# Kernel tuning notes

Measured on AMD Instinct MI355X. Metric: run time of the kernel, lower is better.

Reference implementation:

```python
import jax, jax.numpy as jnp
import numpy as np

B = 1024
N_CPGS = 20000
N_FREQS = N_CPGS // 2 + 1  # 10001
HIDDEN = (256, 128, 64)
LN_EPS = 1e-5


def setup_inputs() -> dict:
    key = jax.random.key(0)
    keys = jax.random.split(key, 16)
    inp = {"x": jax.random.normal(keys[0], (B, N_CPGS), dtype=jnp.float32)}
    in_dim = N_FREQS
    for i, h in enumerate(HIDDEN):
        inp[f"W{i}"] = jax.random.normal(keys[1 + i], (h, in_dim), dtype=jnp.float32) * 0.01
        inp[f"alpha{i}"] = jnp.full((h, in_dim), 0.01, dtype=jnp.float32)
        inp[f"b{i}"] = jnp.zeros((h,), dtype=jnp.float32)
        inp[f"eta{i}"] = jnp.asarray(0.1, dtype=jnp.float32)
        inp[f"g{i}"] = jnp.ones((h,), dtype=jnp.float32)   # LayerNorm gamma
        inp[f"be{i}"] = jnp.zeros((h,), dtype=jnp.float32)  # LayerNorm beta
        in_dim = h
    inp["head_w"] = jax.random.normal(keys[10], (1, in_dim), dtype=jnp.float32) * (1.0 / np.sqrt(in_dim))
    inp["head_b"] = jnp.zeros((1,), dtype=jnp.float32)
    return inp


def _hebbian_layer(x, W, alpha, b, eta):
    # y_slow = x W^T + b;  plastic[b,i] = eta * tanh(y_slow)[b,i] * sum_j sigmoid(alpha)[i,j] * x_norm[b,j] * x[b,j]
    y_slow = jnp.einsum('bd,hd->bh', x, W) + b
    x_norm = x / (jnp.linalg.norm(x, axis=-1, keepdims=True) + 1e-8)
    c = x_norm * x  # (B, in) -- collapses the (B,out,in) outer-product trace algebraically
    plastic = eta * jnp.tanh(y_slow) * jnp.einsum('bd,hd->bh', c, jax.nn.sigmoid(alpha))
    return y_slow + plastic


def _layer_norm(h, g, be):
    mu = jnp.mean(h, axis=-1, keepdims=True)
    var = jnp.mean((h - mu) ** 2, axis=-1, keepdims=True)
    return (h - mu) * jax.lax.rsqrt(var + LN_EPS) * g + be


def reference(x, W0, alpha0, b0, eta0, g0, be0,
              W1, alpha1, b1, eta1, g1, be1,
              W2, alpha2, b2, eta2, g2, be2,
              head_w, head_b):
    # FFT spectral front-end
    xc = x - jnp.mean(x, axis=1, keepdims=True)
    h = jnp.log1p(jnp.abs(jnp.fft.rfft(xc, axis=1)))  # (B, N_FREQS)
    params = [(W0, alpha0, b0, eta0, g0, be0),
              (W1, alpha1, b1, eta1, g1, be1),
              (W2, alpha2, b2, eta2, g2, be2)]
    for (W, a, b, eta, g, be) in params:
        h = jax.nn.gelu(_layer_norm(_hebbian_layer(h, W, a, b, eta), g, be), approximate=False)
        # dropout is identity in eval mode
    return (jnp.einsum('bd,od->bo', h, head_w) + head_b)[:, 0]  # (B,)
```

## Files before the change

### kernel.cpp

```cpp
#include <hip/hip_runtime.h>
#include <hip/hip_bf16.h>
#include <math.h>

typedef short bf16x8 __attribute__((ext_vector_type(8)));
typedef float f32x4 __attribute__((ext_vector_type(4)));

static __device__ __forceinline__ unsigned short f2bf(float f) {
    unsigned int u = __float_as_uint(f);
    unsigned int r = (u + 0x7fffu + ((u >> 16) & 1u)) >> 16;
    return (unsigned short)r;
}

static __device__ __forceinline__ bf16x8 sq_bf16x8(bf16x8 a) {
    bf16x8 r;
    #pragma unroll
    for (int i = 0; i < 8; ++i) {
        unsigned int u = ((unsigned int)(unsigned short)a[i]) << 16;
        float f = __uint_as_float(u);
        f *= f;
        r[i] = (short)f2bf(f);
    }
    return r;
}

static __device__ __forceinline__ float gelu_f(float x) {
    return 0.5f * x * (1.f + erff(x * 0.70710678118654752f));
}

static __device__ __forceinline__ void gload_lds16(const void* g, void* l) {
    __builtin_amdgcn_global_load_lds(
        (const __attribute__((address_space(1))) unsigned int*)g,
        (__attribute__((address_space(3))) unsigned int*)l, 16, 0, 0);
}

static __device__ __forceinline__ int ldsmap(int i) { return i + (i >> 6); }

static __device__ __forceinline__ int rev4(int k) {
    int d0 = k % 10; k /= 10;
    int d1 = k % 10; k /= 10;
    int d2 = k % 10; int d3 = k / 10;
    return d0 * 1000 + d1 * 100 + d2 * 10 + d3;
}

static __device__ __forceinline__ void dft5(
    float a0r, float a0i, float a1r, float a1i, float a2r, float a2i,
    float a3r, float a3i, float a4r, float a4i,
    float* Xr, float* Xi)
{
    const float c1 = 0.30901699437494742f, c2 = -0.80901699437494745f;
    const float s1 = 0.95105651629515357f, s2 = 0.58778525229247312f;
    float t1r = a1r + a4r, t1i = a1i + a4i;
    float d1r = a1r - a4r, d1i = a1i - a4i;
    float t2r = a2r + a3r, t2i = a2i + a3i;
    float d2r = a2r - a3r, d2i = a2i - a3i;
    Xr[0] = a0r + t1r + t2r; Xi[0] = a0i + t1i + t2i;
    float m1r = a0r + c1 * t1r + c2 * t2r, m1i = a0i + c1 * t1i + c2 * t2i;
    float m2r = a0r + c2 * t1r + c1 * t2r, m2i = a0i + c2 * t1i + c1 * t2i;
    float n1r = s1 * d1r + s2 * d2r, n1i = s1 * d1i + s2 * d2i;
    float n2r = s2 * d1r - s1 * d2r, n2i = s2 * d1i - s1 * d2i;
    Xr[1] = m1r + n1i; Xi[1] = m1i - n1r;
    Xr[4] = m1r - n1i; Xi[4] = m1i + n1r;
    Xr[2] = m2r + n2i; Xi[2] = m2i - n2r;
    Xr[3] = m2r - n2i; Xi[3] = m2i + n2r;
}

template<int S>
static __device__ __forceinline__ void radix10_stage(
    float* __restrict__ reb, float* __restrict__ imb, int tid, float mean)
{
    constexpr int L  = (S == 0) ? 1000 : (S == 1) ? 100 : (S == 2) ? 10 : 1;
    constexpr int SC = (S == 0) ? 1 : (S == 1) ? 10 : (S == 2) ? 100 : 1000;
    constexpr bool TW = (S != 3);

    const float WR[5] = {1.f, 0.80901699437494745f, 0.30901699437494742f,
                         -0.30901699437494742f, -0.80901699437494745f};
    const float WI[5] = {0.f, -0.58778525229247312f, -0.95105651629515357f,
                         -0.95105651629515357f, -0.58778525229247312f};

    for (int w = tid; w < 1000; w += 512) {
        int g, j;
        if (S == 0)      { g = 0; j = w; }
        else if (S == 3) { g = w; j = 0; }
        else             { g = w / L; j = w - g * L; }
        const int base = g * (10 * L) + j;

        float ar[10], ai[10];
        #pragma unroll
        for (int u = 0; u < 10; ++u) {
            int idx = ldsmap(base + u * L);
            ar[u] = reb[idx];
            ai[u] = imb[idx];
        }
        if (S == 0) {
            #pragma unroll
            for (int u = 0; u < 10; ++u) { ar[u] -= mean; ai[u] -= mean; }
        }

        float Er[5], Ei[5], Or[5], Oi[5];
        dft5(ar[0], ai[0], ar[2], ai[2], ar[4], ai[4], ar[6], ai[6], ar[8], ai[8], Er, Ei);
        dft5(ar[1], ai[1], ar[3], ai[3], ar[5], ai[5], ar[7], ai[7], ar[9], ai[9], Or, Oi);
        #pragma unroll
        for (int k = 1; k < 5; ++k) {
            float tr = Or[k] * WR[k] - Oi[k] * WI[k];
            Oi[k] = Or[k] * WI[k] + Oi[k] * WR[k];
            Or[k] = tr;
        }

        if (TW) {
            const float ang = (float)(j * SC) * -6.28318530717958648e-4f;
            float w1c, w1s;
            __sincosf(ang, &w1s, &w1c);
            float twr[10], twi[10];
            twr[0] = 1.f; twi[0] = 0.f;
            #pragma unroll
            for (int t = 1; t < 10; ++t) {
                twr[t] = twr[t - 1] * w1c - twi[t - 1] * w1s;
                twi[t] = twr[t - 1] * w1s + twi[t - 1] * w1c;
            }
            #pragma unroll
            for (int k = 0; k < 5; ++k) {
                float xr0 = Er[k] + Or[k], xi0 = Ei[k] + Oi[k];
                float xr1 = Er[k] - Or[k], xi1 = Ei[k] - Oi[k];
                int i0 = ldsmap(base + k * L);
                int i1 = ldsmap(base + (k + 5) * L);
                if (k == 0) {
                    reb[i0] = xr0;
                    imb[i0] = xi0;
                } else {
                    reb[i0] = xr0 * twr[k] - xi0 * twi[k];
                    imb[i0] = xr0 * twi[k] + xi0 * twr[k];
                }
                reb[i1] = xr1 * twr[k + 5] - xi1 * twi[k + 5];
                imb[i1] = xr1 * twi[k + 5] + xi1 * twr[k + 5];
            }
        } else {
            #pragma unroll
            for (int k = 0; k < 5; ++k) {
                int i0 = ldsmap(base + k * L);
                int i1 = ldsmap(base + (k + 5) * L);
                reb[i0] = Er[k] + Or[k]; imb[i0] = Ei[k] + Oi[k];
                reb[i1] = Er[k] - Or[k]; imb[i1] = Ei[k] - Oi[k];
            }
        }
    }
}

__global__ __launch_bounds__(512, 4)
void fft_prep_kernel(const float* __restrict__ x,
                     unsigned short* __restrict__ hb,
                     float* __restrict__ hnorm,
                     const float* __restrict__ W0, const float* __restrict__ A0,
                     unsigned short* __restrict__ Wb, unsigned short* __restrict__ Sb,
                     const float* __restrict__ W1, const float* __restrict__ A1,
                     const float* __restrict__ W2, const float* __restrict__ A2,
                     float* __restrict__ W1T, float* __restrict__ S1T,
                     float* __restrict__ W2T, float* __restrict__ S2T)
{
    if (blockIdx.x >= 1024) {
        int idx = (blockIdx.x - 1024) * 512 + threadIdx.x;
        if (idx < 1280128) {
            const bool isW = idx < 640064;
            const int f4 = isW ? idx : idx - 640064;
            const float* src = isW ? W0 : A0;
            unsigned short* dst = isW ? Wb : Sb;
            float4 v = ((const float4*)src)[f4];
            float e[4] = {v.x, v.y, v.z, v.w};
            int flat = f4 * 4;
            int row = flat / 10001;
            int col = flat - row * 10001;
            #pragma unroll
            for (int i = 0; i < 4; ++i) {
                if (col == 10001) { row++; col = 0; }
                float val = isW ? e[i] : 1.f / (1.f + expf(-e[i]));
                dst[(size_t)row * 10240 + col] = f2bf(val);
                col++;
            }
        } else if (idx < 1341312) {
            int i = idx - 1280128;
            int row = i / 239;
            int col = 10001 + (i - row * 239);
            Wb[(size_t)row * 10240 + col] = 0;
            Sb[(size_t)row * 10240 + col] = 0;
        } else if (idx < 1423232) {
            int o = idx - 1341312;
            if (o < 32768) {
                int d = o >> 7, h = o & 127;
                W1T[o] = W1[h * 256 + d];
            } else if (o < 65536) {
                int p = o - 32768;
                int d = p >> 7, h = p & 127;
                S1T[p] = 1.f / (1.f + expf(-A1[h * 256 + d]));
            } else if (o < 73728) {
                int p = o - 65536;
                int d = p >> 6, h = p & 63;
                W2T[p] = W2[h * 128 + d];
            } else {
                int p = o - 73728;
                int d = p >> 6, h = p & 63;
                S2T[p] = 1.f / (1.f + expf(-A2[h * 128 + d]));
            }
        }
        return;
    }

    __shared__ float reb[10156];
    __shared__ float imb[10156];
    __shared__ float redbuf[8];

    const int b = blockIdx.x;
    const int tid = threadIdx.x;
    const int lane = tid & 63;
    const int wv = tid >> 6;
    const float* xr = x + (size_t)b * 20000;

    float sum = 0.f;
    for (int i4 = tid; i4 < 5000; i4 += 512) {
        float4 v = ((const float4*)xr)[i4];
        sum += v.x + v.y + v.z + v.w;
        int n = i4 * 2;
        reb[ldsmap(n)]     = v.x; imb[ldsmap(n)]     = v.y;
        reb[ldsmap(n + 1)] = v.z; imb[ldsmap(n + 1)] = v.w;
    }
    #pragma unroll
    for (int o = 32; o; o >>= 1) sum += __shfl_xor(sum, o);
    __syncthreads();
    if (lane == 0) redbuf[wv] = sum;
    __syncthreads();
    float tot = 0.f;
    #pragma unroll
    for (int i = 0; i < 8; ++i) tot += redbuf[i];
    const float mean = tot * (1.f / 20000.f);

    radix10_stage<0>(reb, imb, tid, mean);
    __syncthreads();
    radix10_stage<1>(reb, imb, tid, 0.f);
    __syncthreads();
    radix10_stage<2>(reb, imb, tid, 0.f);
    __syncthreads();
    radix10_stage<3>(reb, imb, tid, 0.f);
    __syncthreads();

    float sumsq = 0.f;
    unsigned short* hrow = hb + (size_t)b * 10240;
    #pragma unroll
    for (int i = 0; i < 20; ++i) {
        int k = tid + i * 512;
        float hval = 0.f;
        if (k <= 10000) {
            int k1 = (k == 10000) ? 0 : k;
            int k2 = (10000 - k) % 10000;
            int i1 = ldsmap(rev4(k1));
            int i2 = ldsmap(rev4(k2));
            float zr = reb[i1], zi = imb[i1];
            float wr = reb[i2], wi = imb[i2];
            float er = 0.5f * (zr + wr);
            float ei = 0.5f * (zi - wi);
            float odr = 0.5f * (zi + wi);
            float odi = -0.5f * (zr - wr);
            float ct, st;
            __sincosf((float)k * -3.14159265358979324e-4f, &st, &ct);
            float xre = er + ct * odr - st * odi;
            float xim = ei + ct * odi + st * odr;
            hval = log1pf(sqrtf(xre * xre + xim * xim));
        }
        hrow[k] = f2bf(hval);
        sumsq += hval * hval;
    }
    #pragma unroll
    for (int o = 32; o; o >>= 1) sumsq += __shfl_xor(sumsq, o);
    __syncthreads();
    if (lane == 0) redbuf[wv] = sumsq;
    __syncthreads();
    if (tid == 0) {
        float tsq = 0.f;
        #pragma unroll
        for (int i = 0; i < 8; ++i) tsq += redbuf[i];
        hnorm[b] = 1.f / (sqrtf(tsq) + 1e-8f);
    }
}

__global__ __launch_bounds__(256, 2)
void gemm0_kernel(const unsigned short* __restrict__ hb,
                  const unsigned short* __restrict__ Wb, const unsigned short* __restrict__ Sb,
                  float* __restrict__ Py, float* __restrict__ Pp)
{
    __shared__ unsigned short Ah[128 * 64];
    __shared__ unsigned short Bw[64 * 64];
    __shared__ unsigned short Bs[64 * 64];

    const int t = threadIdx.x;
    const int b0 = blockIdx.x * 128;
    const int n0 = blockIdx.y * 64;
    const int z = blockIdx.z;
    const int lane = t & 63;
    const int wv = t >> 6;
    const int ml = lane & 15;
    const int q4 = lane >> 4;
    const int s0 = q4 ^ (ml & 7);

    const int sub = lane >> 3;
    const int sl = lane & 7;
    const int gsw = sl ^ sub;

    f32x4 accY[2][4], accP[2][4];
    #pragma unroll
    for (int mt = 0; mt < 2; ++mt)
        #pragma unroll
        for (int nt = 0; nt < 4; ++nt) {
            accY[mt][nt] = (f32x4){0.f, 0.f, 0.f, 0.f};
            accP[mt][nt] = (f32x4){0.f, 0.f, 0.f, 0.f};
        }

    const int kbase = z * 640;

    for (int step = 0; step < 10; ++step) {
        const int k0 = kbase + step * 64;
        __syncthreads();
        #pragma unroll
        for (int j = 0; j < 4; ++j) {
            const int c = wv * 4 + j;
            const size_t go = (size_t)(b0 + c * 8 + sub) * 10240 + k0 + gsw * 8;
            gload_lds16(&hb[go], &Ah[c * 512]);
        }
        #pragma unroll
        for (int j = 0; j < 2; ++j) {
            const int c = wv * 2 + j;
            const size_t go = (size_t)(n0 + c * 8 + sub) * 10240 + k0 + gsw * 8;
            gload_lds16(&Wb[go], &Bw[c * 512]);
            gload_lds16(&Sb[go], &Bs[c * 512]);
        }
        __syncthreads();

        #pragma unroll
        for (int kk = 0; kk < 2; ++kk) {
            const int slot = (s0 ^ (kk << 2)) << 3;
            bf16x8 ah[2], ac[2], bw[4], bs[4];
            #pragma unroll
            for (int mt = 0; mt < 2; ++mt) {
                int mrow = wv * 32 + mt * 16 + ml;
                ah[mt] = *(const bf16x8*)&Ah[mrow * 64 + slot];
                ac[mt] = sq_bf16x8(ah[mt]);
            }
            #pragma unroll
            for (int nt = 0; nt < 4; ++nt) {
                int nrow = nt * 16 + ml;
                bw[nt] = *(const bf16x8*)&Bw[nrow * 64 + slot];
                bs[nt] = *(const bf16x8*)&Bs[nrow * 64 + slot];
            }
            #pragma unroll
            for (int mt = 0; mt < 2; ++mt)
                #pragma unroll
                for (int nt = 0; nt < 4; ++nt) {
                    accY[mt][nt] = __builtin_amdgcn_mfma_f32_16x16x32_bf16(ah[mt], bw[nt], accY[mt][nt], 0, 0, 0);
                    accP[mt][nt] = __builtin_amdgcn_mfma_f32_16x16x32_bf16(ac[mt], bs[nt], accP[mt][nt], 0, 0, 0);
                }
        }
    }

    const int rq = q4 * 4;
    #pragma unroll
    for (int mt = 0; mt < 2; ++mt)
        #pragma unroll
        for (int nt = 0; nt < 4; ++nt)
            #pragma unroll
            for (int r = 0; r < 4; ++r) {
                int m = b0 + wv * 32 + mt * 16 + rq + r;
                int n = n0 + nt * 16 + ml;
                size_t o = ((size_t)z * 1024 + m) * 256 + n;
                Py[o] = accY[mt][nt][r];
                Pp[o] = accP[mt][nt][r];
            }
}

__global__ __launch_bounds__(256)
void combine0_kernel(const float* __restrict__ Py, const float* __restrict__ Pp,
                     const float* __restrict__ hnorm,
                     const float* __restrict__ b0v, const float* __restrict__ eta0p,
                     const float* __restrict__ g0, const float* __restrict__ be0,
                     float* __restrict__ h1, float* __restrict__ c1)
{
    __shared__ float red[4];
    const int b = blockIdx.x;
    const int h = threadIdx.x;
    const int lane = h & 63;
    const int wv = h >> 6;

    float ys = 0.f, ps = 0.f;
    for (int s = 0; s < 16; ++s) {
        size_t o = ((size_t)s * 1024 + b) * 256 + h;
        ys += Py[o];
        ps += Pp[o];
    }
    ps *= hnorm[b];
    float y = ys + b0v[h];
    float v = y + eta0p[0] * tanhf(y) * ps;

    float s1 = v;
    #pragma unroll
    for (int o = 32; o; o >>= 1) s1 += __shfl_xor(s1, o);
    __syncthreads();
    if (lane == 0) red[wv] = s1;
    __syncthreads();
    float sum = red[0] + red[1] + red[2] + red[3];

    float s2 = v * v;
    #pragma unroll
    for (int o = 32; o; o >>= 1) s2 += __shfl_xor(s2, o);
    __syncthreads();
    if (lane == 0) red[wv] = s2;
    __syncthreads();
    float sumsq = red[0] + red[1] + red[2] + red[3];

    float mu = sum * (1.f / 256.f);
    float var = sumsq * (1.f / 256.f) - mu * mu;
    float u = (v - mu) * rsqrtf(var + 1e-5f) * g0[h] + be0[h];
    float gl = gelu_f(u);

    float s3 = gl * gl;
    #pragma unroll
    for (int o = 32; o; o >>= 1) s3 += __shfl_xor(s3, o);
    __syncthreads();
    if (lane == 0) red[wv] = s3;
    __syncthreads();
    float gsq = red[0] + red[1] + red[2] + red[3];
    float inv = 1.f / (sqrtf(gsq) + 1e-8f);

    h1[(size_t)b * 256 + h] = gl;
    c1[(size_t)b * 256 + h] = gl * gl * inv;
}

__global__ __launch_bounds__(256)
void tail_kernel(const float* __restrict__ h1, const float* __restrict__ c1,
                 const float* __restrict__ W1T, const float* __restrict__ S1T,
                 const float* __restrict__ b1, const float* __restrict__ eta1p,
                 const float* __restrict__ g1, const float* __restrict__ be1,
                 const float* __restrict__ W2T, const float* __restrict__ S2T,
                 const float* __restrict__ b2, const float* __restrict__ eta2p,
                 const float* __restrict__ g2, const float* __restrict__ be2,
                 const float* __restrict__ hw, const float* __restrict__ hbod,
                 float* __restrict__ out)
{
    __shared__ float sh[4][256];
    __shared__ float sc[4][256];
    __shared__ float sv[4][128];
    __shared__ float sh2[4][128];
    __shared__ float sc2[4][128];
    __shared__ float sv2[4][64];

    const int t = threadIdx.x;
    const int b0 = blockIdx.x * 4;
    const int lane = t & 63;
    const int wv = t >> 6;

    #pragma unroll
    for (int i = 0; i < 4; ++i) {
        int idx = t + i * 256;
        int r = idx >> 8, d = idx & 255;
        sh[r][d] = h1[(size_t)(b0 + r) * 256 + d];
        sc[r][d] = c1[(size_t)(b0 + r) * 256 + d];
    }
    __syncthreads();

    const int hcol = t & 127;
    const int r2 = t >> 7;
    float ya[2] = {0.f, 0.f};
    float pa[2] = {0.f, 0.f};
    for (int d = 0; d < 256; ++d) {
        float w = W1T[d * 128 + hcol];
        float s = S1T[d * 128 + hcol];
        #pragma unroll
        for (int i = 0; i < 2; ++i) {
            int r = r2 * 2 + i;
            ya[i] += sh[r][d] * w;
            pa[i] += sc[r][d] * s;
        }
    }
    const float e1 = eta1p[0];
    #pragma unroll
    for (int i = 0; i < 2; ++i) {
        int r = r2 * 2 + i;
        float y = ya[i] + b1[hcol];
        sv[r][hcol] = y + e1 * tanhf(y) * pa[i];
    }
    __syncthreads();

    {
        int r = wv;
        float v0 = sv[r][lane];
        float v1 = sv[r][lane + 64];
        float s = v0 + v1, sq = v0 * v0 + v1 * v1;
        #pragma unroll
        for (int o = 32; o; o >>= 1) { s += __shfl_xor(s, o); sq += __shfl_xor(sq, o); }
        float mu = s * (1.f / 128.f);
        float var = sq * (1.f / 128.f) - mu * mu;
        float rs = rsqrtf(var + 1e-5f);
        float u0 = (v0 - mu) * rs * g1[lane] + be1[lane];
        float u1 = (v1 - mu) * rs * g1[lane + 64] + be1[lane + 64];
        float ge0 = gelu_f(u0);
        float ge1 = gelu_f(u1);
        float gsq = ge0 * ge0 + ge1 * ge1;
        #pragma unroll
        for (int o = 32; o; o >>= 1) gsq += __shfl_xor(gsq, o);
        float inv = 1.f / (sqrtf(gsq) + 1e-8f);
        sh2[r][lane] = ge0; sh2[r][lane + 64] = ge1;
        sc2[r][lane] = ge0 * ge0 * inv; sc2[r][lane + 64] = ge1 * ge1 * inv;
    }
    __syncthreads();

    const int h2c = t & 63;
    const int r4 = t >> 6;
    float yb = 0.f, pb = 0.f;
    for (int d = 0; d < 128; ++d) {
        yb += sh2[r4][d] * W2T[d * 64 + h2c];
        pb += sc2[r4][d] * S2T[d * 64 + h2c];
    }
    {
        const float e2 = eta2p[0];
        float y = yb + b2[h2c];
        sv2[r4][h2c] = y + e2 * tanhf(y) * pb;
    }
    __syncthreads();

    {
        int r = wv;
        float v0 = sv2[r][lane];
        float s = v0, sq = v0 * v0;
        #pragma unroll
        for (int o = 32; o; o >>= 1) { s += __shfl_xor(s, o); sq += __shfl_xor(sq, o); }
        float mu = s * (1.f / 64.f);
        float var = sq * (1.f / 64.f) - mu * mu;
        float rs = rsqrtf(var + 1e-5f);
        float u = (v0 - mu) * rs * g2[lane] + be2[lane];
        float g = gelu_f(u);
        float hc = g * hw[lane];
        #pragma unroll
        for (int o = 32; o; o >>= 1) hc += __shfl_xor(hc, o);
        if (lane == 0) out[b0 + r] = hc + hbod[0];
    }
}

extern "C" void kernel_launch(void* const* d_in, const int* in_sizes, int n_in,
                              void* d_out, int out_size, void* d_ws, size_t ws_size,
                              hipStream_t stream)
{
    const float* x    = (const float*)d_in[0];
    const float* W0   = (const float*)d_in[1];
    const float* A0   = (const float*)d_in[2];
    const float* b0   = (const float*)d_in[3];
    const float* eta0 = (const float*)d_in[4];
    const float* g0   = (const float*)d_in[5];
    const float* be0  = (const float*)d_in[6];
    const float* W1   = (const float*)d_in[7];
    const float* A1   = (const float*)d_in[8];
    const float* b1   = (const float*)d_in[9];
    const float* eta1 = (const float*)d_in[10];
    const float* g1   = (const float*)d_in[11];
    const float* be1  = (const float*)d_in[12];
    const float* W2   = (const float*)d_in[13];
    const float* A2   = (const float*)d_in[14];
    const float* b2   = (const float*)d_in[15];
    const float* eta2 = (const float*)d_in[16];
    const float* g2   = (const float*)d_in[17];
    const float* be2  = (const float*)d_in[18];
    const float* hw   = (const float*)d_in[19];
    const float* hbod = (const float*)d_in[20];
    float* out = (float*)d_out;

    char* w = (char*)d_ws;
    unsigned short* hb  = (unsigned short*)(w + 0);
    unsigned short* Wb0 = (unsigned short*)(w + 20971520);
    unsigned short* Sb0 = (unsigned short*)(w + 26214400);
    float* Py   = (float*)(w + 31457280);
    float* Pp   = (float*)(w + 48234496);
    float* h1   = (float*)(w + 65011712);
    float* c1   = (float*)(w + 66060288);
    float* W1T  = (float*)(w + 67108864);
    float* S1T  = (float*)(w + 67239936);
    float* W2T  = (float*)(w + 67371008);
    float* S2T  = (float*)(w + 67403776);
    float* hnm  = (float*)(w + 67436544);

    hipLaunchKernelGGL(fft_prep_kernel, dim3(3804), dim3(512), 0, stream,
                       x, hb, hnm, W0, A0, Wb0, Sb0, W1, A1, W2, A2, W1T, S1T, W2T, S2T);
    hipLaunchKernelGGL(gemm0_kernel, dim3(8, 4, 16), dim3(256), 0, stream, hb, Wb0, Sb0, Py, Pp);
    hipLaunchKernelGGL(combine0_kernel, dim3(1024), dim3(256), 0, stream, Py, Pp, hnm, b0, eta0, g0, be0, h1, c1);
    hipLaunchKernelGGL(tail_kernel, dim3(256), dim3(256), 0, stream, h1, c1, W1T, S1T, b1, eta1, g1, be1,
                       W2T, S2T, b2, eta2, g2, be2, hw, hbod, out);
}
```

Baseline: 282.2 us.

## Process two FFT rows per 1024-thread block, sharing twiddles and index math

The FFT prep kernel now handles two batch rows per block of 1024 threads. Each of the 1000 active threads computes one butterfly position for both rows, so twiddle sincos, twiddle recurrences and LDS index maps are computed once and reused across the rows. The post-processing step also shares its sincos and indices across the two rows. The cost is double the shared memory per block (about 160 KB) and more register pressure, which can lower occupancy, and the side blocks for weight conversion now also run 1024 threads.

After: 294.0 us. 4.2% more time.

```diff
diff --git a/kernel.cpp b/kernel.cpp
--- a/kernel.cpp
+++ b/kernel.cpp
@@ -65,8 +65,9 @@
 }
 
 template<int S>
-static __device__ __forceinline__ void radix10_stage(
-    float* __restrict__ reb, float* __restrict__ imb, int tid, float mean)
+static __device__ __forceinline__ void radix10_stage2(
+    float (*__restrict__ reb)[10156], float (*__restrict__ imb)[10156],
+    int w, float mean0, float mean1)
 {
     constexpr int L  = (S == 0) ? 1000 : (S == 1) ? 100 : (S == 2) ? 10 : 1;
     constexpr int SC = (S == 0) ? 1 : (S == 1) ? 10 : (S == 2) ? 100 : 1000;
@@ -77,23 +78,37 @@
     const float WI[5] = {0.f, -0.58778525229247312f, -0.95105651629515357f,
                          -0.95105651629515357f, -0.58778525229247312f};
 
-    for (int w = tid; w < 1000; w += 512) {
-        int g, j;
-        if (S == 0)      { g = 0; j = w; }
-        else if (S == 3) { g = w; j = 0; }
-        else             { g = w / L; j = w - g * L; }
-        const int base = g * (10 * L) + j;
-
+    int g, j;
+    if (S == 0)      { g = 0; j = w; }
+    else if (S == 3) { g = w; j = 0; }
+    else             { g = w / L; j = w - g * L; }
+    const int base = g * (10 * L) + j;
+
+    int idx[10];
+    #pragma unroll
+    for (int u = 0; u < 10; ++u) idx[u] = ldsmap(base + u * L);
+
+    float twr[10], twi[10];
+    if (TW) {
+        const float ang = (float)(j * SC) * -6.28318530717958648e-4f;
+        float w1c, w1s;
+        __sincosf(ang, &w1s, &w1c);
+        twr[0] = 1.f; twi[0] = 0.f;
+        #pragma unroll
+        for (int t = 1; t < 10; ++t) {
+            twr[t] = twr[t - 1] * w1c - twi[t - 1] * w1s;
+            twi[t] = twr[t - 1] * w1s + twi[t - 1] * w1c;
+        }
+    }
+
+    #pragma unroll
+    for (int r = 0; r < 2; ++r) {
+        const float mm = (S == 0) ? (r ? mean1 : mean0) : 0.f;
         float ar[10], ai[10];
         #pragma unroll
         for (int u = 0; u < 10; ++u) {
-            int idx = ldsmap(base + u * L);
-            ar[u] = reb[idx];
-            ai[u] = imb[idx];
-        }
-        if (S == 0) {
-            #pragma unroll
-            for (int u = 0; u < 10; ++u) { ar[u] -= mean; ai[u] -= mean; }
+            ar[u] = reb[r][idx[u]] - mm;
+            ai[u] = imb[r][idx[u]] - mm;
         }
 
         float Er[5], Ei[5], Or[5], Oi[5];
@@ -107,45 +122,31 @@
         }
 
         if (TW) {
-            const float ang = (float)(j * SC) * -6.28318530717958648e-4f;
-            float w1c, w1s;
-            __sincosf(ang, &w1s, &w1c);
-            float twr[10], twi[10];
-            twr[0] = 1.f; twi[0] = 0.f;
-            #pragma unroll
-            for (int t = 1; t < 10; ++t) {
-                twr[t] = twr[t - 1] * w1c - twi[t - 1] * w1s;
-                twi[t] = twr[t - 1] * w1s + twi[t - 1] * w1c;
-            }
             #pragma unroll
             for (int k = 0; k < 5; ++k) {
                 float xr0 = Er[k] + Or[k], xi0 = Ei[k] + Oi[k];
                 float xr1 = Er[k] - Or[k], xi1 = Ei[k] - Oi[k];
-                int i0 = ldsmap(base + k * L);
-                int i1 = ldsmap(base + (k + 5) * L);
                 if (k == 0) {
-                    reb[i0] = xr0;
-                    imb[i0] = xi0;
+                    reb[r][idx[0]] = xr0;
+                    imb[r][idx[0]] = xi0;
                 } else {
-                    reb[i0] = xr0 * twr[k] - xi0 * twi[k];
-                    imb[i0] = xr0 * twi[k] + xi0 * twr[k];
+                    reb[r][idx[k]] = xr0 * twr[k] - xi0 * twi[k];
+                    imb[r][idx[k]] = xr0 * twi[k] + xi0 * twr[k];
                 }
-                reb[i1] = xr1 * twr[k + 5] - xi1 * twi[k + 5];
-                imb[i1] = xr1 * twi[k + 5] + xi1 * twr[k + 5];
+                reb[r][idx[k + 5]] = xr1 * twr[k + 5] - xi1 * twi[k + 5];
+                imb[r][idx[k + 5]] = xr1 * twi[k + 5] + xi1 * twr[k + 5];
             }
         } else {
             #pragma unroll
             for (int k = 0; k < 5; ++k) {
-                int i0 = ldsmap(base + k * L);
-                int i1 = ldsmap(base + (k + 5) * L);
-                reb[i0] = Er[k] + Or[k]; imb[i0] = Ei[k] + Oi[k];
-                reb[i1] = Er[k] - Or[k]; imb[i1] = Ei[k] - Oi[k];
-            }
-        }
-    }
-}
-
-__global__ __launch_bounds__(512, 4)
+                reb[r][idx[k]]     = Er[k] + Or[k]; imb[r][idx[k]]     = Ei[k] + Oi[k];
+                reb[r][idx[k + 5]] = Er[k] - Or[k]; imb[r][idx[k + 5]] = Ei[k] - Oi[k];
+            }
+        }
+    }
+}
+
+__global__ __launch_bounds__(1024)
 void fft_prep_kernel(const float* __restrict__ x,
                      unsigned short* __restrict__ hb,
                      float* __restrict__ hnorm,
@@ -156,8 +157,8 @@
                      float* __restrict__ W1T, float* __restrict__ S1T,
                      float* __restrict__ W2T, float* __restrict__ S2T)
 {
-    if (blockIdx.x >= 1024) {
-        int idx = (blockIdx.x - 1024) * 512 + threadIdx.x;
+    if (blockIdx.x >= 512) {
+        int idx = (blockIdx.x - 512) * 1024 + threadIdx.x;
         if (idx < 1280128) {
             const bool isW = idx < 640064;
             const int f4 = isW ? idx : idx - 640064;
@@ -203,79 +204,106 @@
         return;
     }
 
-    __shared__ float reb[10156];
-    __shared__ float imb[10156];
-    __shared__ float redbuf[8];
-
-    const int b = blockIdx.x;
+    __shared__ float reb[2][10156];
+    __shared__ float imb[2][10156];
+    __shared__ float redbuf[32];
+
     const int tid = threadIdx.x;
     const int lane = tid & 63;
     const int wv = tid >> 6;
-    const float* xr = x + (size_t)b * 20000;
-
+    const int half = tid >> 9;
+    const int t2 = tid & 511;
+    const int b0 = blockIdx.x * 2;
+
+    const float* xr = x + (size_t)(b0 + half) * 20000;
     float sum = 0.f;
-    for (int i4 = tid; i4 < 5000; i4 += 512) {
+    for (int i4 = t2; i4 < 5000; i4 += 512) {
         float4 v = ((const float4*)xr)[i4];
         sum += v.x + v.y + v.z + v.w;
         int n = i4 * 2;
-        reb[ldsmap(n)]     = v.x; imb[ldsmap(n)]     = v.y;
-        reb[ldsmap(n + 1)] = v.z; imb[ldsmap(n + 1)] = v.w;
+        reb[half][ldsmap(n)]     = v.x; imb[half][ldsmap(n)]     = v.y;
+        reb[half][ldsmap(n + 1)] = v.z; imb[half][ldsmap(n + 1)] = v.w;
     }
     #pragma unroll
     for (int o = 32; o; o >>= 1) sum += __shfl_xor(sum, o);
     __syncthreads();
     if (lane == 0) redbuf[wv] = sum;
     __syncthreads();
-    float tot = 0.f;
-    #pragma unroll
-    for (int i = 0; i < 8; ++i) tot += redbuf[i];
-    const float mean = tot * (1.f / 20000.f);
-
-    radix10_stage<0>(reb, imb, tid, mean);
-    __syncthreads();
-    radix10_stage<1>(reb, imb, tid, 0.f);
-    __syncthreads();
-    radix10_stage<2>(reb, imb, tid, 0.f);
-    __syncthreads();
-    radix10_stage<3>(reb, imb, tid, 0.f);
-    __syncthreads();
-
-    float sumsq = 0.f;
-    unsigned short* hrow = hb + (size_t)b * 10240;
-    #pragma unroll
-    for (int i = 0; i < 20; ++i) {
-        int k = tid + i * 512;
-        float hval = 0.f;
+    float tot0 = 0.f, tot1 = 0.f;
+    #pragma unroll
+    for (int i = 0; i < 8; ++i) { tot0 += redbuf[i]; tot1 += redbuf[8 + i]; }
+    const float mean0 = tot0 * (1.f / 20000.f);
+    const float mean1 = tot1 * (1.f / 20000.f);
+
+    if (tid < 1000) radix10_stage2<0>(reb, imb, tid, mean0, mean1);
+    __syncthreads();
+    if (tid < 1000) radix10_stage2<1>(reb, imb, tid, 0.f, 0.f);
+    __syncthreads();
+    if (tid < 1000) radix10_stage2<2>(reb, imb, tid, 0.f, 0.f);
+    __syncthreads();
+    if (tid < 1000) radix10_stage2<3>(reb, imb, tid, 0.f, 0.f);
+    __syncthreads();
+
+    float sq0 = 0.f, sq1 = 0.f;
+    unsigned short* hrow0 = hb + (size_t)b0 * 10240;
+    unsigned short* hrow1 = hrow0 + 10240;
+    #pragma unroll
+    for (int i = 0; i < 10; ++i) {
+        int k = tid + i * 1024;
         if (k <= 10000) {
             int k1 = (k == 10000) ? 0 : k;
-            int k2 = (10000 - k) % 10000;
+            int k2 = (10000 - k1) % 10000;
             int i1 = ldsmap(rev4(k1));
             int i2 = ldsmap(rev4(k2));
-            float zr = reb[i1], zi = imb[i1];
-            float wr = reb[i2], wi = imb[i2];
-            float er = 0.5f * (zr + wr);
-            float ei = 0.5f * (zi - wi);
-            float odr = 0.5f * (zi + wi);
-            float odi = -0.5f * (zr - wr);
             float ct, st;
             __sincosf((float)k * -3.14159265358979324e-4f, &st, &ct);
-            float xre = er + ct * odr - st * odi;
-            float xim = ei + ct * odi + st * odr;
-            hval = log1pf(sqrtf(xre * xre + xim * xim));
-        }
-        hrow[k] = f2bf(hval);
-        sumsq += hval * hval;
-    }
-    #pragma unroll
-    for (int o = 32; o; o >>= 1) sumsq += __shfl_xor(sumsq, o);
-    __syncthreads();
-    if (lane == 0) redbuf[wv] = sumsq;
+
+            {
+                float zr = reb[0][i1], zi = imb[0][i1];
+                float wr = reb[0][i2], wi = imb[0][i2];
+                float er = 0.5f * (zr + wr);
+                float ei = 0.5f * (zi - wi);
+                float odr = 0.5f * (zi + wi);
+                float odi = -0.5f * (zr - wr);
+                float xre = er + ct * odr - st * odi;
+                float xim = ei + ct * odi + st * odr;
+                float hv = log1pf(sqrtf(xre * xre + xim * xim));
+                hrow0[k] = f2bf(hv);
+                sq0 += hv * hv;
+            }
+            {
+                float zr = reb[1][i1], zi = imb[1][i1];
+                float wr = reb[1][i2], wi = imb[1][i2];
+                float er = 0.5f * (zr + wr);
+                float ei = 0.5f * (zi - wi);
+                float odr = 0.5f * (zi + wi);
+                float odi = -0.5f * (zr - wr);
+                float xre = er + ct * odr - st * odi;
+                float xim = ei + ct * odi + st * odr;
+                float hv = log1pf(sqrtf(xre * xre + xim * xim));
+                hrow1[k] = f2bf(hv);
+                sq1 += hv * hv;
+            }
+        } else {
+            hrow0[k] = 0;
+            hrow1[k] = 0;
+        }
+    }
+    #pragma unroll
+    for (int o = 32; o; o >>= 1) { sq0 += __shfl_xor(sq0, o); sq1 += __shfl_xor(sq1, o); }
+    __syncthreads();
+    if (lane == 0) { redbuf[wv] = sq0; redbuf[16 + wv] = sq1; }
     __syncthreads();
     if (tid == 0) {
-        float tsq = 0.f;
-        #pragma unroll
-        for (int i = 0; i < 8; ++i) tsq += redbuf[i];
-        hnorm[b] = 1.f / (sqrtf(tsq) + 1e-8f);
+        float t = 0.f;
+        #pragma unroll
+        for (int i = 0; i < 16; ++i) t += redbuf[i];
+        hnorm[b0] = 1.f / (sqrtf(t) + 1e-8f);
+    } else if (tid == 1) {
+        float t = 0.f;
+        #pragma unroll
+        for (int i = 0; i < 16; ++i) t += redbuf[16 + i];
+        hnorm[b0 + 1] = 1.f / (sqrtf(t) + 1e-8f);
     }
 }
 
@@ -580,7 +608,7 @@
     float* S2T  = (float*)(w + 67403776);
     float* hnm  = (float*)(w + 67436544);
 
-    hipLaunchKernelGGL(fft_prep_kernel, dim3(3804), dim3(512), 0, stream,
+    hipLaunchKernelGGL(fft_prep_kernel, dim3(1902), dim3(1024), 0, stream,
                        x, hb, hnm, W0, A0, Wb0, Sb0, W1, A1, W2, A2, W1T, S1T, W2T, S2T);
     hipLaunchKernelGGL(gemm0_kernel, dim3(8, 4, 16), dim3(256), 0, stream, hb, Wb0, Sb0, Py, Pp);
     hipLaunchKernelGGL(combine0_kernel, dim3(1024), dim3(256), 0, stream, Py, Pp, hnm, b0, eta0, g0, be0, h1, c1);
```

## Fuse layer-0 combine into tail kernel and use cheaper log in FFT

Applied to the files above, without the earlier changes.

Merges the split-K reduction, Hebbian combine, LayerNorm and GELU for layer 0 into the tail kernel. Each block now handles four rows, which removes one launch and the h1/c1 round trip through global memory. The FFT epilogue swaps the modulo for a branch and log1pf for __logf(1+x). The fused kernel uses only 256 blocks to read the split-K partials, and __logf(1+x) loses precision for small magnitudes.

Measured after the change: 266.0 us. 1.06x faster.

```diff
diff --git a/kernel.cpp b/kernel.cpp
--- a/kernel.cpp
+++ b/kernel.cpp
@@ -248,7 +248,7 @@
         float hval = 0.f;
         if (k <= 10000) {
             int k1 = (k == 10000) ? 0 : k;
-            int k2 = (10000 - k) % 10000;
+            int k2 = (k1 == 0) ? 0 : 10000 - k1;
             int i1 = ldsmap(rev4(k1));
             int i2 = ldsmap(rev4(k2));
             float zr = reb[i1], zi = imb[i1];
@@ -261,7 +261,7 @@
             __sincosf((float)k * -3.14159265358979324e-4f, &st, &ct);
             float xre = er + ct * odr - st * odi;
             float xim = ei + ct * odi + st * odr;
-            hval = log1pf(sqrtf(xre * xre + xim * xim));
+            hval = __logf(1.f + sqrtf(xre * xre + xim * xim));
         }
         hrow[k] = f2bf(hval);
         sumsq += hval * hval;
@@ -373,64 +373,10 @@
 }
 
 __global__ __launch_bounds__(256)
-void combine0_kernel(const float* __restrict__ Py, const float* __restrict__ Pp,
-                     const float* __restrict__ hnorm,
-                     const float* __restrict__ b0v, const float* __restrict__ eta0p,
-                     const float* __restrict__ g0, const float* __restrict__ be0,
-                     float* __restrict__ h1, float* __restrict__ c1)
-{
-    __shared__ float red[4];
-    const int b = blockIdx.x;
-    const int h = threadIdx.x;
-    const int lane = h & 63;
-    const int wv = h >> 6;
-
-    float ys = 0.f, ps = 0.f;
-    for (int s = 0; s < 16; ++s) {
-        size_t o = ((size_t)s * 1024 + b) * 256 + h;
-        ys += Py[o];
-        ps += Pp[o];
-    }
-    ps *= hnorm[b];
-    float y = ys + b0v[h];
-    float v = y + eta0p[0] * tanhf(y) * ps;
-
-    float s1 = v;
-    #pragma unroll
-    for (int o = 32; o; o >>= 1) s1 += __shfl_xor(s1, o);
-    __syncthreads();
-    if (lane == 0) red[wv] = s1;
-    __syncthreads();
-    float sum = red[0] + red[1] + red[2] + red[3];
-
-    float s2 = v * v;
-    #pragma unroll
-    for (int o = 32; o; o >>= 1) s2 += __shfl_xor(s2, o);
-    __syncthreads();
-    if (lane == 0) red[wv] = s2;
-    __syncthreads();
-    float sumsq = red[0] + red[1] + red[2] + red[3];
-
-    float mu = sum * (1.f / 256.f);
-    float var = sumsq * (1.f / 256.f) - mu * mu;
-    float u = (v - mu) * rsqrtf(var + 1e-5f) * g0[h] + be0[h];
-    float gl = gelu_f(u);
-
-    float s3 = gl * gl;
-    #pragma unroll
-    for (int o = 32; o; o >>= 1) s3 += __shfl_xor(s3, o);
-    __syncthreads();
-    if (lane == 0) red[wv] = s3;
-    __syncthreads();
-    float gsq = red[0] + red[1] + red[2] + red[3];
-    float inv = 1.f / (sqrtf(gsq) + 1e-8f);
-
-    h1[(size_t)b * 256 + h] = gl;
-    c1[(size_t)b * 256 + h] = gl * gl * inv;
-}
-
-__global__ __launch_bounds__(256)
-void tail_kernel(const float* __restrict__ h1, const float* __restrict__ c1,
+void combine_tail_kernel(const float* __restrict__ Py, const float* __restrict__ Pp,
+                 const float* __restrict__ hnorm,
+                 const float* __restrict__ b0v, const float* __restrict__ eta0p,
+                 const float* __restrict__ g0, const float* __restrict__ be0,
                  const float* __restrict__ W1T, const float* __restrict__ S1T,
                  const float* __restrict__ b1, const float* __restrict__ eta1p,
                  const float* __restrict__ g1, const float* __restrict__ be1,
@@ -446,18 +392,70 @@
     __shared__ float sh2[4][128];
     __shared__ float sc2[4][128];
     __shared__ float sv2[4][64];
+    __shared__ float redA[4][4];
+    __shared__ float redB[4][4];
 
     const int t = threadIdx.x;
     const int b0 = blockIdx.x * 4;
     const int lane = t & 63;
     const int wv = t >> 6;
 
-    #pragma unroll
-    for (int i = 0; i < 4; ++i) {
-        int idx = t + i * 256;
-        int r = idx >> 8, d = idx & 255;
-        sh[r][d] = h1[(size_t)(b0 + r) * 256 + d];
-        sc[r][d] = c1[(size_t)(b0 + r) * 256 + d];
+    const float e0 = eta0p[0];
+    const float bias0 = b0v[t];
+    float v[4];
+    #pragma unroll
+    for (int r = 0; r < 4; ++r) {
+        float ys = 0.f, ps = 0.f;
+        #pragma unroll 4
+        for (int s = 0; s < 16; ++s) {
+            size_t o = ((size_t)s * 1024 + b0 + r) * 256 + t;
+            ys += Py[o];
+            ps += Pp[o];
+        }
+        ps *= hnorm[b0 + r];
+        float y = ys + bias0;
+        v[r] = y + e0 * tanhf(y) * ps;
+    }
+
+    float s1[4], s2[4];
+    #pragma unroll
+    for (int r = 0; r < 4; ++r) { s1[r] = v[r]; s2[r] = v[r] * v[r]; }
+    #pragma unroll
+    for (int o = 32; o; o >>= 1)
+        #pragma unroll
+        for (int r = 0; r < 4; ++r) { s1[r] += __shfl_xor(s1[r], o); s2[r] += __shfl_xor(s2[r], o); }
+    if (lane == 0)
+        #pragma unroll
+        for (int r = 0; r < 4; ++r) { redA[wv][r] = s1[r]; redB[wv][r] = s2[r]; }
+    __syncthreads();
+
+    const float gg = g0[t], bb = be0[t];
+    float gl[4], s3[4];
+    #pragma unroll
+    for (int r = 0; r < 4; ++r) {
+        float sum = redA[0][r] + redA[1][r] + redA[2][r] + redA[3][r];
+        float sumsq = redB[0][r] + redB[1][r] + redB[2][r] + redB[3][r];
+        float mu = sum * (1.f / 256.f);
+        float var = sumsq * (1.f / 256.f) - mu * mu;
+        float u = (v[r] - mu) * rsqrtf(var + 1e-5f) * gg + bb;
+        gl[r] = gelu_f(u);
+        s3[r] = gl[r] * gl[r];
+    }
+    #pragma unroll
+    for (int o = 32; o; o >>= 1)
+        #pragma unroll
+        for (int r = 0; r < 4; ++r) s3[r] += __shfl_xor(s3[r], o);
+    __syncthreads();
+    if (lane == 0)
+        #pragma unroll
+        for (int r = 0; r < 4; ++r) redA[wv][r] = s3[r];
+    __syncthreads();
+    #pragma unroll
+    for (int r = 0; r < 4; ++r) {
+        float gsq = redA[0][r] + redA[1][r] + redA[2][r] + redA[3][r];
+        float inv = 1.f / (sqrtf(gsq) + 1e-8f);
+        sh[r][t] = gl[r];
+        sc[r][t] = gl[r] * gl[r] * inv;
     }
     __syncthreads();
 
@@ -572,18 +570,16 @@
     unsigned short* Sb0 = (unsigned short*)(w + 26214400);
     float* Py   = (float*)(w + 31457280);
     float* Pp   = (float*)(w + 48234496);
-    float* h1   = (float*)(w + 65011712);
-    float* c1   = (float*)(w + 66060288);
-    float* W1T  = (float*)(w + 67108864);
-    float* S1T  = (float*)(w + 67239936);
-    float* W2T  = (float*)(w + 67371008);
-    float* S2T  = (float*)(w + 67403776);
-    float* hnm  = (float*)(w + 67436544);
+    float* W1T  = (float*)(w + 65011712);
+    float* S1T  = (float*)(w + 65142784);
+    float* W2T  = (float*)(w + 65273856);
+    float* S2T  = (float*)(w + 65306624);
+    float* hnm  = (float*)(w + 65339392);
 
     hipLaunchKernelGGL(fft_prep_kernel, dim3(3804), dim3(512), 0, stream,
                        x, hb, hnm, W0, A0, Wb0, Sb0, W1, A1, W2, A2, W1T, S1T, W2T, S2T);
     hipLaunchKernelGGL(gemm0_kernel, dim3(8, 4, 16), dim3(256), 0, stream, hb, Wb0, Sb0, Py, Pp);
-    hipLaunchKernelGGL(combine0_kernel, dim3(1024), dim3(256), 0, stream, Py, Pp, hnm, b0, eta0, g0, be0, h1, c1);
-    hipLaunchKernelGGL(tail_kernel, dim3(256), dim3(256), 0, stream, h1, c1, W1T, S1T, b1, eta1, g1, be1,
+    hipLaunchKernelGGL(combine_tail_kernel, dim3(256), dim3(256), 0, stream, Py, Pp, hnm,
+                       b0, eta0, g0, be0, W1T, S1T, b1, eta1, g1, be1,
                        W2T, S2T, b2, eta2, g2, be2, hw, hbod, out);
 }
```
